# Performance work log

Hardware: AMD Instinct MI355X
Metric: run time of the kernel (lower is better)

## Reference

```python
import jax, jax.numpy as jnp
import numpy as np

B, N, D, P = 4, 4096, 64, 2
M, H = 64, 128
ARENA = 20.0  # positions uniform in [0, ARENA]^2; radius 1.0 -> ~32 neighbors


def _mlp2(x, Wa, ba, Wb, bb):
    return jax.nn.relu(x @ Wa + ba) @ Wb + bb


def setup_inputs() -> dict:
    key = jax.random.key(0)
    ks = jax.random.split(key, 14)
    def lin(k, fan_in, fan_out):
        bound = 1.0 / np.sqrt(fan_in)
        kw, kb = jax.random.split(k)
        W = jax.random.uniform(kw, (fan_in, fan_out), jnp.float32, -bound, bound)
        b = jax.random.uniform(kb, (fan_out,), jnp.float32, -bound, bound)
        return W, b
    W1, b1 = lin(ks[0], D, H)
    W2, b2 = lin(ks[1], H, M)
    W3, b3 = lin(ks[2], 2 * M, H)
    W4, b4 = lin(ks[3], H, M)
    W5, b5 = lin(ks[4], D + M, H)
    W6, b6 = lin(ks[5], H, D)
    agent_states = jax.random.normal(ks[6], (B, N, D), jnp.float32)
    agent_positions = jax.random.uniform(ks[7], (B, N, P), jnp.float32) * ARENA
    return {
        "agent_states": agent_states,
        "agent_positions": agent_positions,
        "neighbor_radius": 1,
        "W1": W1, "b1": b1, "W2": W2, "b2": b2,
        "W3": W3, "b3": b3, "W4": W4, "b4": b4,
        "W5": W5, "b5": b5, "W6": W6, "b6": b6,
    }


def reference(agent_states, agent_positions, neighbor_radius,
              W1, b1, W2, b2, W3, b3, W4, b4, W5, b5, W6, b6):
    n = agent_states.shape[1]
    # message encoder MLP: [B,N,D] -> [B,N,M]
    messages = _mlp2(agent_states, W1, b1, W2, b2)
    # dense pairwise distances [B,N,N] (faithful to original O(N^2) mask)
    diff = agent_positions[:, :, None, :] - agent_positions[:, None, :, :]
    distances = jnp.sqrt(jnp.sum(diff * diff, axis=-1))
    adj = (distances < jnp.float32(neighbor_radius)).astype(messages.dtype)
    adj = adj * (1.0 - jnp.eye(n, dtype=messages.dtype))[None]
    deg = jnp.clip(jnp.sum(adj, axis=-1, keepdims=True), 1.0, None)
    adj = adj / deg
    # vectorized form of the per-agent gather-aggregate loop
    aggregated = jnp.einsum('bij,bjm->bim', adj, messages)
    combined = jnp.concatenate([messages, aggregated], axis=-1)
    final_msgs = _mlp2(combined, W3, b3, W4, b4)
    feats = jnp.concatenate([agent_states, final_msgs], axis=-1)
    out = _mlp2(feats, W5, b5, W6, b6)
    return agent_states + out
```

## Files before the change

### kernel.cpp

```cpp
#include <hip/hip_runtime.h>

typedef unsigned short u16;
typedef __bf16 bf16x8 __attribute__((ext_vector_type(8)));
typedef unsigned short ushort8 __attribute__((ext_vector_type(8)));
typedef float f32x4 __attribute__((ext_vector_type(4)));

#define DEV_INLINE __device__ __forceinline__

constexpr int NB = 4;
constexpr int NAG = 4096;
constexpr int ROWS = NB * NAG;
constexpr int GRID = 20;
constexpr int CELLS = GRID * GRID;
constexpr int CSTRIDE = 404;
constexpr int MAXNB = 320;

DEV_INLINE u16 f2bu(float x) { __bf16 h = (__bf16)x; return __builtin_bit_cast(u16, h); }
DEV_INLINE float bu2f(u16 u) { return __builtin_bit_cast(float, ((unsigned)u) << 16); }

__global__ __launch_bounds__(1024) void setup_kernel(
    const float* __restrict__ pos,
    const float* __restrict__ W1, const float* __restrict__ W2,
    const float* __restrict__ W3, const float* __restrict__ W4,
    const float* __restrict__ W5, const float* __restrict__ W6,
    u16* __restrict__ wts, float2* __restrict__ pos_sorted,
    int* __restrict__ cell_start, int* __restrict__ sid, int* __restrict__ invp)
{
  if (blockIdx.x >= NB) {
    const int idx = (blockIdx.x - NB) * 1024 + threadIdx.x;
    const float* src; int n, k, Nc;
    if (idx < 8192)       { src = W1; int li = idx;          n = li >> 6; k = li & 63;  Nc = 128; }
    else if (idx < 16384) { src = W2; int li = idx - 8192;   n = li >> 7; k = li & 127; Nc = 64;  }
    else if (idx < 32768) { src = W3; int li = idx - 16384;  n = li >> 7; k = li & 127; Nc = 128; }
    else if (idx < 40960) { src = W4; int li = idx - 32768;  n = li >> 7; k = li & 127; Nc = 64;  }
    else if (idx < 57344) { src = W5; int li = idx - 40960;  n = li >> 7; k = li & 127; Nc = 128; }
    else                  { src = W6; int li = idx - 57344;  n = li >> 7; k = li & 127; Nc = 64;  }
    wts[idx] = f2bu(src[k * Nc + n]);
    return;
  }

  __shared__ int cnt_s[CELLS];
  __shared__ int start_s[CELLS + 1];
  __shared__ int scan_s[512];
  __shared__ u16 cell_of[NAG];
  __shared__ u16 rank_of[NAG];

  const int b = blockIdx.x;
  const float2* pb = (const float2*)(pos + (size_t)b * NAG * 2);
  for (int c = threadIdx.x; c < CELLS; c += 1024) cnt_s[c] = 0;
  __syncthreads();

  for (int i = threadIdx.x; i < NAG; i += 1024) {
    float2 p = pb[i];
    int cx = min(max((int)floorf(p.x), 0), GRID - 1);
    int cy = min(max((int)floorf(p.y), 0), GRID - 1);
    int c = cy * GRID + cx;
    int rk = atomicAdd(&cnt_s[c], 1);
    cell_of[i] = (u16)c;
    rank_of[i] = (u16)rk;
  }
  __syncthreads();

  if (threadIdx.x < 512) scan_s[threadIdx.x] = (threadIdx.x < CELLS) ? cnt_s[threadIdx.x] : 0;
  __syncthreads();
  for (int off = 1; off < 512; off <<= 1) {
    int x = 0;
    if (threadIdx.x < 512) {
      x = scan_s[threadIdx.x];
      if (threadIdx.x >= off) x += scan_s[threadIdx.x - off];
    }
    __syncthreads();
    if (threadIdx.x < 512) scan_s[threadIdx.x] = x;
    __syncthreads();
  }
  if (threadIdx.x <= CELLS) {
    int st = (threadIdx.x == 0) ? 0 : scan_s[threadIdx.x - 1];
    start_s[threadIdx.x] = st;
    cell_start[b * CSTRIDE + threadIdx.x] = st;
  }
  __syncthreads();

  for (int i = threadIdx.x; i < NAG; i += 1024) {
    int k = start_s[cell_of[i]] + rank_of[i];
    sid[b * NAG + k]  = b * NAG + i;
    invp[b * NAG + i] = b * NAG + k;
    pos_sorted[b * NAG + k] = pb[i];
  }
}

template<bool BF>
DEV_INLINE bf16x8 loadA(const void* __restrict__ src, int row, int c) {
  if constexpr (BF) {
    ushort8 u = *reinterpret_cast<const ushort8*>((const u16*)src + (size_t)row * 64 + c);
    return __builtin_bit_cast(bf16x8, u);
  } else {
    const float* f = (const float*)src + (size_t)row * 64 + c;
    f32x4 a = *(const f32x4*)f;
    f32x4 b = *(const f32x4*)(f + 4);
    bf16x8 r;
    r[0] = (__bf16)a[0]; r[1] = (__bf16)a[1]; r[2] = (__bf16)a[2]; r[3] = (__bf16)a[3];
    r[4] = (__bf16)b[0]; r[5] = (__bf16)b[1]; r[6] = (__bf16)b[2]; r[7] = (__bf16)b[3];
    return r;
  }
}

template<int KIN, bool A0BF, bool A1BF, bool RESID, bool OUTBF, bool PERM>
__global__ __launch_bounds__(256) void mlp_mfma(
    const void* __restrict__ src0, const void* __restrict__ src1,
    const u16* __restrict__ WaT, const u16* __restrict__ WbT,
    const float* __restrict__ ba, const float* __restrict__ bb,
    const float* __restrict__ resid, const int* __restrict__ perm,
    void* __restrict__ dst)
{
  constexpr int KP = KIN + 8;
  extern __shared__ u16 smem[];
  u16* WaTs = smem;
  u16* WbTs = smem + 128 * KP;
  const int lane = threadIdx.x & 63;
  const int wave = threadIdx.x >> 6;
  u16* hs = WbTs + 64 * 136 + wave * (16 * 136);

  for (int t = threadIdx.x; t < (128 * KIN) / 8; t += 256) {
    int e = t * 8; int n = e / KIN; int k = e - n * KIN;
    *(ushort8*)&WaTs[n * KP + k] = *(const ushort8*)&WaT[e];
  }
  for (int t = threadIdx.x; t < 1024; t += 256) {
    int e = t * 8; int n = e >> 7; int k = e & 127;
    *(ushort8*)&WbTs[n * 136 + k] = *(const ushort8*)&WbT[e];
  }
  __syncthreads();

  const int l15 = lane & 15;
  const int khalf = (lane >> 4) * 8;
  const int rb = blockIdx.x * 64 + wave * 16;
  const int row = rb + l15;

  f32x4 acc1[8] = {};
#pragma unroll
  for (int kt = 0; kt < KIN / 32; ++kt) {
    const int cc = (kt & 1) * 32 + khalf;
    bf16x8 a;
    if constexpr (KIN == 128) {
      if (kt >= 2) a = loadA<A1BF>(src1, row, cc);
      else         a = loadA<A0BF>(src0, row, cc);
    } else {
      a = loadA<A0BF>(src0, row, cc);
    }
#pragma unroll
    for (int nt = 0; nt < 8; ++nt) {
      ushort8 bu = *(const ushort8*)&WaTs[(nt * 16 + l15) * KP + kt * 32 + khalf];
      acc1[nt] = __builtin_amdgcn_mfma_f32_16x16x32_bf16(
          a, __builtin_bit_cast(bf16x8, bu), acc1[nt], 0, 0, 0);
    }
  }

#pragma unroll
  for (int nt = 0; nt < 8; ++nt) {
    const float bav = ba[nt * 16 + l15];
#pragma unroll
    for (int r = 0; r < 4; ++r) {
      float v = acc1[nt][r] + bav;
      v = fmaxf(v, 0.0f);
      hs[((lane >> 4) * 4 + r) * 136 + nt * 16 + l15] = f2bu(v);
    }
  }

  f32x4 acc2[4] = {};
#pragma unroll
  for (int kt = 0; kt < 4; ++kt) {
    ushort8 au = *(const ushort8*)&hs[l15 * 136 + kt * 32 + khalf];
    bf16x8 a2 = __builtin_bit_cast(bf16x8, au);
#pragma unroll
    for (int nt = 0; nt < 4; ++nt) {
      ushort8 bu = *(const ushort8*)&WbTs[(nt * 16 + l15) * 136 + kt * 32 + khalf];
      acc2[nt] = __builtin_amdgcn_mfma_f32_16x16x32_bf16(
          a2, __builtin_bit_cast(bf16x8, bu), acc2[nt], 0, 0, 0);
    }
  }

  int drow[4];
#pragma unroll
  for (int r = 0; r < 4; ++r) {
    const int orow = rb + (lane >> 4) * 4 + r;
    drow[r] = PERM ? perm[orow] : orow;
  }

#pragma unroll
  for (int nt = 0; nt < 4; ++nt) {
    const int gc = nt * 16 + l15;
    const float bbv = bb[gc];
#pragma unroll
    for (int r = 0; r < 4; ++r) {
      const int m = (lane >> 4) * 4 + r;
      const size_t o = (size_t)drow[r] * 64 + gc;
      float v = acc2[nt][r] + bbv;
      if constexpr (RESID) v += resid[(size_t)(rb + m) * 64 + gc];
      if constexpr (OUTBF) ((u16*)dst)[o] = f2bu(v);
      else                 ((float*)dst)[o] = v;
    }
  }
}

__global__ __launch_bounds__(256) void agg_kernel(
    const float2* __restrict__ pos_sorted, const u16* __restrict__ msgs,
    const int* __restrict__ cell_start, const int* __restrict__ radius_ptr,
    u16* __restrict__ aggr)
{
  __shared__ u16 idxb[4][MAXNB];
  const int b = blockIdx.y;
  const int lane = threadIdx.x & 63;
  const int wave = threadIdx.x >> 6;
  const int k = blockIdx.x * 4 + wave;
  const float2* pb = pos_sorted + (size_t)b * NAG;
  const float2 pk = pb[k];
  const float r = (float)(*radius_ptr);
  const float r2 = __fmul_rn(r, r);
  const int cx = min(max((int)floorf(pk.x), 0), GRID - 1);
  const int cy = min(max((int)floorf(pk.y), 0), GRID - 1);
  const int* cs = cell_start + b * CSTRIDE;
  const unsigned long long lt = (1ull << lane) - 1ull;

  int cnt = 0;
#pragma unroll
  for (int dy = -1; dy <= 1; ++dy) {
    const int yy = cy + dy;
    if (yy < 0 || yy >= GRID) continue;
    const int x0 = max(cx - 1, 0), x1 = min(cx + 1, GRID - 1);
    const int c0 = cs[yy * GRID + x0];
    const int c1 = cs[yy * GRID + x1 + 1];
    for (int base = c0; base < c1; base += 64) {
      const int j = base + lane;
      bool ok = false;
      if (j < c1) {
        const float2 pj = pb[j];
        const float dx_ = pk.x - pj.x;
        const float dy_ = pk.y - pj.y;
        const float d2 = __fadd_rn(__fmul_rn(dx_, dx_), __fmul_rn(dy_, dy_));
        ok = (d2 < r2) && (j != k);
      }
      const unsigned long long m = __ballot(ok);
      if (ok) {
        const int p = cnt + __popcll(m & lt);
        if (p < MAXNB) idxb[wave][p] = (u16)j;
      }
      cnt += (int)__popcll(m);
    }
  }

  const u16* mb = msgs + (size_t)b * NAG * 64;
  float acc = 0.0f;
  const int n = min(cnt, MAXNB);
  for (int g = 0; g < n; g += 8) {
    ushort8 ii = *(const ushort8*)&idxb[wave][g];
    float vs[8];
#pragma unroll
    for (int s = 0; s < 8; ++s) {
      const int jj = (g + s < n) ? (int)ii[s] : (int)ii[0];
      vs[s] = bu2f(mb[(size_t)jj * 64 + lane]);
    }
#pragma unroll
    for (int s = 0; s < 8; ++s) acc += (g + s < n) ? vs[s] : 0.0f;
  }
  const float inv = 1.0f / (float)(cnt > 0 ? cnt : 1);
  aggr[((size_t)b * NAG + k) * 64 + lane] = f2bu(acc * inv);
}

extern "C" void kernel_launch(void* const* d_in, const int* in_sizes, int n_in,
                              void* d_out, int out_size, void* d_ws, size_t ws_size,
                              hipStream_t stream) {
  const float* states = (const float*)d_in[0];
  const float* pos    = (const float*)d_in[1];
  const int*   radius = (const int*)d_in[2];
  const float* W1 = (const float*)d_in[3];
  const float* b1 = (const float*)d_in[4];
  const float* W2 = (const float*)d_in[5];
  const float* b2 = (const float*)d_in[6];
  const float* W3 = (const float*)d_in[7];
  const float* b3 = (const float*)d_in[8];
  const float* W4 = (const float*)d_in[9];
  const float* b4 = (const float*)d_in[10];
  const float* W5 = (const float*)d_in[11];
  const float* b5 = (const float*)d_in[12];
  const float* W6 = (const float*)d_in[13];
  const float* b6 = (const float*)d_in[14];
  float* out = (float*)d_out;

  u16* ws16   = (u16*)d_ws;
  u16* msgs   = ws16;
  u16* aggr   = msgs + (size_t)ROWS * 64;
  u16* finalm = aggr + (size_t)ROWS * 64;
  u16* wts    = finalm + (size_t)ROWS * 64;
  char* pbyte = (char*)(wts + 65536);
  float2* pos_sorted = (float2*)pbyte;
  int* cell_start = (int*)(pbyte + (size_t)ROWS * 8);
  int* sid  = cell_start + NB * CSTRIDE;
  int* invp = sid + ROWS;

  constexpr int LDS64  = (128 * 72  + 64 * 136 + 4 * 16 * 136) * 2;
  constexpr int LDS128 = (128 * 136 + 64 * 136 + 4 * 16 * 136) * 2;

  setup_kernel<<<NB + 64, 1024, 0, stream>>>(
      pos, W1, W2, W3, W4, W5, W6, wts, pos_sorted, cell_start, sid, invp);

  mlp_mfma<64, false, false, false, true, true><<<256, 256, LDS64, stream>>>(
      states, nullptr, wts + 0, wts + 8192, b1, b2, nullptr, invp, msgs);

  agg_kernel<<<dim3(NAG / 4, NB), 256, 0, stream>>>(
      pos_sorted, msgs, cell_start, radius, aggr);

  mlp_mfma<128, true, true, false, true, true><<<256, 256, LDS128, stream>>>(
      msgs, aggr, wts + 16384, wts + 32768, b3, b4, nullptr, sid, finalm);

  mlp_mfma<128, false, true, true, false, false><<<256, 256, LDS128, stream>>>(
      states, finalm, wts + 40960, wts + 57344, b5, b6, states, nullptr, out);
}
```

Before: 50.03 us.

## Fuse setup with first MLP and merge final two MLPs into one kernel

The standalone setup kernel is merged into the first MLP launch as extra blocks: spatial binning uses a wave-shuffle scan, and W1/W2 are converted to bf16 directly in LDS. The message buffer stays in original agent order, and the aggregation kernel maps sorted neighbor indices back through sid. The last two MLPs become one kernel that keeps the intermediate final messages in LDS, which removes a launch and the finalm global round trip. In exchange, the fused MLP kernel needs much more LDS, which may lower occupancy, and the gathers in aggregation lose the locality the sorted message order gave them.

```diff
diff --git a/kernel.cpp b/kernel.cpp
--- a/kernel.cpp
+++ b/kernel.cpp
@@ -18,74 +18,9 @@
 DEV_INLINE u16 f2bu(float x) { __bf16 h = (__bf16)x; return __builtin_bit_cast(u16, h); }
 DEV_INLINE float bu2f(u16 u) { return __builtin_bit_cast(float, ((unsigned)u) << 16); }
 
-__global__ __launch_bounds__(1024) void setup_kernel(
-    const float* __restrict__ pos,
-    const float* __restrict__ W1, const float* __restrict__ W2,
-    const float* __restrict__ W3, const float* __restrict__ W4,
-    const float* __restrict__ W5, const float* __restrict__ W6,
-    u16* __restrict__ wts, float2* __restrict__ pos_sorted,
-    int* __restrict__ cell_start, int* __restrict__ sid, int* __restrict__ invp)
-{
-  if (blockIdx.x >= NB) {
-    const int idx = (blockIdx.x - NB) * 1024 + threadIdx.x;
-    const float* src; int n, k, Nc;
-    if (idx < 8192)       { src = W1; int li = idx;          n = li >> 6; k = li & 63;  Nc = 128; }
-    else if (idx < 16384) { src = W2; int li = idx - 8192;   n = li >> 7; k = li & 127; Nc = 64;  }
-    else if (idx < 32768) { src = W3; int li = idx - 16384;  n = li >> 7; k = li & 127; Nc = 128; }
-    else if (idx < 40960) { src = W4; int li = idx - 32768;  n = li >> 7; k = li & 127; Nc = 64;  }
-    else if (idx < 57344) { src = W5; int li = idx - 40960;  n = li >> 7; k = li & 127; Nc = 128; }
-    else                  { src = W6; int li = idx - 57344;  n = li >> 7; k = li & 127; Nc = 64;  }
-    wts[idx] = f2bu(src[k * Nc + n]);
-    return;
-  }
-
-  __shared__ int cnt_s[CELLS];
-  __shared__ int start_s[CELLS + 1];
-  __shared__ int scan_s[512];
-  __shared__ u16 cell_of[NAG];
-  __shared__ u16 rank_of[NAG];
-
-  const int b = blockIdx.x;
-  const float2* pb = (const float2*)(pos + (size_t)b * NAG * 2);
-  for (int c = threadIdx.x; c < CELLS; c += 1024) cnt_s[c] = 0;
-  __syncthreads();
-
-  for (int i = threadIdx.x; i < NAG; i += 1024) {
-    float2 p = pb[i];
-    int cx = min(max((int)floorf(p.x), 0), GRID - 1);
-    int cy = min(max((int)floorf(p.y), 0), GRID - 1);
-    int c = cy * GRID + cx;
-    int rk = atomicAdd(&cnt_s[c], 1);
-    cell_of[i] = (u16)c;
-    rank_of[i] = (u16)rk;
-  }
-  __syncthreads();
-
-  if (threadIdx.x < 512) scan_s[threadIdx.x] = (threadIdx.x < CELLS) ? cnt_s[threadIdx.x] : 0;
-  __syncthreads();
-  for (int off = 1; off < 512; off <<= 1) {
-    int x = 0;
-    if (threadIdx.x < 512) {
-      x = scan_s[threadIdx.x];
-      if (threadIdx.x >= off) x += scan_s[threadIdx.x - off];
-    }
-    __syncthreads();
-    if (threadIdx.x < 512) scan_s[threadIdx.x] = x;
-    __syncthreads();
-  }
-  if (threadIdx.x <= CELLS) {
-    int st = (threadIdx.x == 0) ? 0 : scan_s[threadIdx.x - 1];
-    start_s[threadIdx.x] = st;
-    cell_start[b * CSTRIDE + threadIdx.x] = st;
-  }
-  __syncthreads();
-
-  for (int i = threadIdx.x; i < NAG; i += 1024) {
-    int k = start_s[cell_of[i]] + rank_of[i];
-    sid[b * NAG + k]  = b * NAG + i;
-    invp[b * NAG + i] = b * NAG + k;
-    pos_sorted[b * NAG + k] = pb[i];
-  }
+DEV_INLINE f32x4 MF(bf16x8 a, const u16* p, f32x4 c) {
+  ushort8 bu = *(const ushort8*)p;
+  return __builtin_amdgcn_mfma_f32_16x16x32_bf16(a, __builtin_bit_cast(bf16x8, bu), c, 0, 0, 0);
 }
 
 template<bool BF>
@@ -104,107 +39,138 @@
   }
 }
 
-template<int KIN, bool A0BF, bool A1BF, bool RESID, bool OUTBF, bool PERM>
-__global__ __launch_bounds__(256) void mlp_mfma(
-    const void* __restrict__ src0, const void* __restrict__ src1,
-    const u16* __restrict__ WaT, const u16* __restrict__ WbT,
-    const float* __restrict__ ba, const float* __restrict__ bb,
-    const float* __restrict__ resid, const int* __restrict__ perm,
-    void* __restrict__ dst)
+__global__ __launch_bounds__(256) void fused_setup_mlp1(
+    const float* __restrict__ pos, const float* __restrict__ states,
+    const float* __restrict__ W1, const float* __restrict__ b1,
+    const float* __restrict__ W2, const float* __restrict__ b2,
+    const float* __restrict__ W3, const float* __restrict__ W4,
+    const float* __restrict__ W5, const float* __restrict__ W6,
+    u16* __restrict__ wts, u16* __restrict__ msgs,
+    float2* __restrict__ pos_sorted, int* __restrict__ cell_start,
+    int* __restrict__ sid)
 {
-  constexpr int KP = KIN + 8;
   extern __shared__ u16 smem[];
+  const int tid = threadIdx.x;
+  const int lane = tid & 63;
+  const int wave = tid >> 6;
+
+  if (blockIdx.x < NB) {
+    int* cnt_s = (int*)smem;
+    int* start_s = cnt_s + CELLS;
+    u16* cell_of = (u16*)(start_s + CELLS + 1);
+    u16* rank_of = cell_of + NAG;
+    const int b = blockIdx.x;
+    const float2* pb = (const float2*)(pos + (size_t)b * NAG * 2);
+    for (int c = tid; c < CELLS; c += 256) cnt_s[c] = 0;
+    __syncthreads();
+    for (int i = tid; i < NAG; i += 256) {
+      float2 p = pb[i];
+      int cx = min(max((int)floorf(p.x), 0), GRID - 1);
+      int cy = min(max((int)floorf(p.y), 0), GRID - 1);
+      int c = cy * GRID + cx;
+      rank_of[i] = (u16)atomicAdd(&cnt_s[c], 1);
+      cell_of[i] = (u16)c;
+    }
+    __syncthreads();
+    if (wave == 0) {
+      int carry = 0;
+      for (int g = 0; g < CELLS; g += 64) {
+        int c = g + lane;
+        int x = (c < CELLS) ? cnt_s[c] : 0;
+#pragma unroll
+        for (int off = 1; off < 64; off <<= 1) {
+          int y = __shfl_up(x, off, 64);
+          if (lane >= off) x += y;
+        }
+        if (c < CELLS) start_s[c + 1] = carry + x;
+        carry += __shfl(x, 63, 64);
+      }
+      if (lane == 0) start_s[0] = 0;
+    }
+    __syncthreads();
+    for (int c = tid; c <= CELLS; c += 256) cell_start[b * CSTRIDE + c] = start_s[c];
+    for (int i = tid; i < NAG; i += 256) {
+      int kk = start_s[cell_of[i]] + (int)rank_of[i];
+      sid[b * NAG + kk] = b * NAG + i;
+      pos_sorted[b * NAG + kk] = pb[i];
+    }
+    return;
+  }
+
+  if (blockIdx.x >= NB + 256) {
+    const int base = (blockIdx.x - (NB + 256)) * 3072;
+#pragma unroll
+    for (int t = 0; t < 12; ++t) {
+      int idx = base + t * 256 + tid;
+      const float* src; int n, k, Nc;
+      if (idx < 16384)      { src = W3; n = idx >> 7; k = idx & 127; Nc = 128; }
+      else if (idx < 24576) { int li = idx - 16384; src = W4; n = li >> 7; k = li & 127; Nc = 64; }
+      else if (idx < 40960) { int li = idx - 24576; src = W5; n = li >> 7; k = li & 127; Nc = 128; }
+      else                  { int li = idx - 40960; src = W6; n = li >> 7; k = li & 127; Nc = 64; }
+      wts[idx] = f2bu(src[k * Nc + n]);
+    }
+    return;
+  }
+
   u16* WaTs = smem;
-  u16* WbTs = smem + 128 * KP;
-  const int lane = threadIdx.x & 63;
-  const int wave = threadIdx.x >> 6;
+  u16* WbTs = smem + 128 * 72;
   u16* hs = WbTs + 64 * 136 + wave * (16 * 136);
 
-  for (int t = threadIdx.x; t < (128 * KIN) / 8; t += 256) {
-    int e = t * 8; int n = e / KIN; int k = e - n * KIN;
-    *(ushort8*)&WaTs[n * KP + k] = *(const ushort8*)&WaT[e];
-  }
-  for (int t = threadIdx.x; t < 1024; t += 256) {
-    int e = t * 8; int n = e >> 7; int k = e & 127;
-    *(ushort8*)&WbTs[n * 136 + k] = *(const ushort8*)&WbT[e];
+  for (int e = tid; e < 64 * 128; e += 256) {
+    int n = e & 127, k = e >> 7;
+    WaTs[n * 72 + k] = f2bu(W1[e]);
+  }
+  for (int e = tid; e < 128 * 64; e += 256) {
+    int n = e & 63, k = e >> 6;
+    WbTs[n * 136 + k] = f2bu(W2[e]);
   }
   __syncthreads();
 
   const int l15 = lane & 15;
   const int khalf = (lane >> 4) * 8;
-  const int rb = blockIdx.x * 64 + wave * 16;
+  const int rb = (blockIdx.x - NB) * 64 + wave * 16;
   const int row = rb + l15;
 
   f32x4 acc1[8] = {};
 #pragma unroll
-  for (int kt = 0; kt < KIN / 32; ++kt) {
-    const int cc = (kt & 1) * 32 + khalf;
-    bf16x8 a;
-    if constexpr (KIN == 128) {
-      if (kt >= 2) a = loadA<A1BF>(src1, row, cc);
-      else         a = loadA<A0BF>(src0, row, cc);
-    } else {
-      a = loadA<A0BF>(src0, row, cc);
-    }
-#pragma unroll
-    for (int nt = 0; nt < 8; ++nt) {
-      ushort8 bu = *(const ushort8*)&WaTs[(nt * 16 + l15) * KP + kt * 32 + khalf];
-      acc1[nt] = __builtin_amdgcn_mfma_f32_16x16x32_bf16(
-          a, __builtin_bit_cast(bf16x8, bu), acc1[nt], 0, 0, 0);
-    }
-  }
-
+  for (int kt = 0; kt < 2; ++kt) {
+    bf16x8 a = loadA<false>(states, row, kt * 32 + khalf);
+#pragma unroll
+    for (int nt = 0; nt < 8; ++nt)
+      acc1[nt] = MF(a, &WaTs[(nt * 16 + l15) * 72 + kt * 32 + khalf], acc1[nt]);
+  }
 #pragma unroll
   for (int nt = 0; nt < 8; ++nt) {
-    const float bav = ba[nt * 16 + l15];
-#pragma unroll
-    for (int r = 0; r < 4; ++r) {
-      float v = acc1[nt][r] + bav;
-      v = fmaxf(v, 0.0f);
-      hs[((lane >> 4) * 4 + r) * 136 + nt * 16 + l15] = f2bu(v);
-    }
-  }
-
+    const float bav = b1[nt * 16 + l15];
+#pragma unroll
+    for (int r = 0; r < 4; ++r)
+      hs[((lane >> 4) * 4 + r) * 136 + nt * 16 + l15] = f2bu(fmaxf(acc1[nt][r] + bav, 0.0f));
+  }
   f32x4 acc2[4] = {};
 #pragma unroll
   for (int kt = 0; kt < 4; ++kt) {
     ushort8 au = *(const ushort8*)&hs[l15 * 136 + kt * 32 + khalf];
     bf16x8 a2 = __builtin_bit_cast(bf16x8, au);
 #pragma unroll
-    for (int nt = 0; nt < 4; ++nt) {
-      ushort8 bu = *(const ushort8*)&WbTs[(nt * 16 + l15) * 136 + kt * 32 + khalf];
-      acc2[nt] = __builtin_amdgcn_mfma_f32_16x16x32_bf16(
-          a2, __builtin_bit_cast(bf16x8, bu), acc2[nt], 0, 0, 0);
-    }
-  }
-
-  int drow[4];
-#pragma unroll
-  for (int r = 0; r < 4; ++r) {
-    const int orow = rb + (lane >> 4) * 4 + r;
-    drow[r] = PERM ? perm[orow] : orow;
-  }
-
+    for (int nt = 0; nt < 4; ++nt)
+      acc2[nt] = MF(a2, &WbTs[(nt * 16 + l15) * 136 + kt * 32 + khalf], acc2[nt]);
+  }
 #pragma unroll
   for (int nt = 0; nt < 4; ++nt) {
     const int gc = nt * 16 + l15;
-    const float bbv = bb[gc];
+    const float bbv = b2[gc];
 #pragma unroll
     for (int r = 0; r < 4; ++r) {
       const int m = (lane >> 4) * 4 + r;
-      const size_t o = (size_t)drow[r] * 64 + gc;
-      float v = acc2[nt][r] + bbv;
-      if constexpr (RESID) v += resid[(size_t)(rb + m) * 64 + gc];
-      if constexpr (OUTBF) ((u16*)dst)[o] = f2bu(v);
-      else                 ((float*)dst)[o] = v;
+      msgs[(size_t)(rb + m) * 64 + gc] = f2bu(acc2[nt][r] + bbv);
     }
   }
 }
 
 __global__ __launch_bounds__(256) void agg_kernel(
     const float2* __restrict__ pos_sorted, const u16* __restrict__ msgs,
-    const int* __restrict__ cell_start, const int* __restrict__ radius_ptr,
-    u16* __restrict__ aggr)
+    const int* __restrict__ cell_start, const int* __restrict__ sid,
+    const int* __restrict__ radius_ptr, u16* __restrict__ aggr)
 {
   __shared__ u16 idxb[4][MAXNB];
   const int b = blockIdx.y;
@@ -218,6 +184,7 @@
   const int cx = min(max((int)floorf(pk.x), 0), GRID - 1);
   const int cy = min(max((int)floorf(pk.y), 0), GRID - 1);
   const int* cs = cell_start + b * CSTRIDE;
+  const int* sb = sid + b * NAG;
   const unsigned long long lt = (1ull << lane) - 1ull;
 
   int cnt = 0;
@@ -241,13 +208,12 @@
       const unsigned long long m = __ballot(ok);
       if (ok) {
         const int p = cnt + __popcll(m & lt);
-        if (p < MAXNB) idxb[wave][p] = (u16)j;
+        if (p < MAXNB) idxb[wave][p] = (u16)sb[j];
       }
       cnt += (int)__popcll(m);
     }
   }
 
-  const u16* mb = msgs + (size_t)b * NAG * 64;
   float acc = 0.0f;
   const int n = min(cnt, MAXNB);
   for (int g = 0; g < n; g += 8) {
@@ -256,13 +222,123 @@
 #pragma unroll
     for (int s = 0; s < 8; ++s) {
       const int jj = (g + s < n) ? (int)ii[s] : (int)ii[0];
-      vs[s] = bu2f(mb[(size_t)jj * 64 + lane]);
+      vs[s] = bu2f(msgs[(size_t)jj * 64 + lane]);
     }
 #pragma unroll
     for (int s = 0; s < 8; ++s) acc += (g + s < n) ? vs[s] : 0.0f;
   }
   const float inv = 1.0f / (float)(cnt > 0 ? cnt : 1);
-  aggr[((size_t)b * NAG + k) * 64 + lane] = f2bu(acc * inv);
+  const int orow = sb[k];
+  aggr[(size_t)orow * 64 + lane] = f2bu(acc * inv);
+}
+
+__global__ __launch_bounds__(256) void mlp23_kernel(
+    const float* __restrict__ states, const u16* __restrict__ msgs,
+    const u16* __restrict__ aggr, const u16* __restrict__ wts,
+    const float* __restrict__ b3, const float* __restrict__ b4,
+    const float* __restrict__ b5, const float* __restrict__ b6,
+    float* __restrict__ out)
+{
+  extern __shared__ u16 smem[];
+  u16* W3s = smem;
+  u16* W4s = W3s + 128 * 136;
+  u16* W5s = W4s + 64 * 136;
+  u16* W6s = W5s + 128 * 136;
+  const int tid = threadIdx.x;
+  const int lane = tid & 63;
+  const int wave = tid >> 6;
+  u16* hs = W6s + 64 * 136 + wave * (2 * 16 * 136);
+  u16* fs = hs + 16 * 136;
+
+  for (int t = tid; t < 2048; t += 256) { int e = t * 8; int n = e >> 7, k = e & 127;
+    *(ushort8*)&W3s[n * 136 + k] = *(const ushort8*)&wts[e]; }
+  for (int t = tid; t < 1024; t += 256) { int e = t * 8; int n = e >> 7, k = e & 127;
+    *(ushort8*)&W4s[n * 136 + k] = *(const ushort8*)&wts[16384 + e]; }
+  for (int t = tid; t < 2048; t += 256) { int e = t * 8; int n = e >> 7, k = e & 127;
+    *(ushort8*)&W5s[n * 136 + k] = *(const ushort8*)&wts[24576 + e]; }
+  for (int t = tid; t < 1024; t += 256) { int e = t * 8; int n = e >> 7, k = e & 127;
+    *(ushort8*)&W6s[n * 136 + k] = *(const ushort8*)&wts[40960 + e]; }
+  __syncthreads();
+
+  const int l15 = lane & 15;
+  const int khalf = (lane >> 4) * 8;
+  const int rb = blockIdx.x * 64 + wave * 16;
+  const int row = rb + l15;
+
+  f32x4 acc1[8] = {};
+#pragma unroll
+  for (int kt = 0; kt < 4; ++kt) {
+    const int cc = (kt & 1) * 32 + khalf;
+    bf16x8 a = (kt < 2) ? loadA<true>(msgs, row, cc) : loadA<true>(aggr, row, cc);
+#pragma unroll
+    for (int nt = 0; nt < 8; ++nt)
+      acc1[nt] = MF(a, &W3s[(nt * 16 + l15) * 136 + kt * 32 + khalf], acc1[nt]);
+  }
+#pragma unroll
+  for (int nt = 0; nt < 8; ++nt) {
+    const float bv = b3[nt * 16 + l15];
+#pragma unroll
+    for (int r = 0; r < 4; ++r)
+      hs[((lane >> 4) * 4 + r) * 136 + nt * 16 + l15] = f2bu(fmaxf(acc1[nt][r] + bv, 0.0f));
+  }
+  f32x4 acc2[4] = {};
+#pragma unroll
+  for (int kt = 0; kt < 4; ++kt) {
+    ushort8 au = *(const ushort8*)&hs[l15 * 136 + kt * 32 + khalf];
+    bf16x8 a2 = __builtin_bit_cast(bf16x8, au);
+#pragma unroll
+    for (int nt = 0; nt < 4; ++nt)
+      acc2[nt] = MF(a2, &W4s[(nt * 16 + l15) * 136 + kt * 32 + khalf], acc2[nt]);
+  }
+#pragma unroll
+  for (int nt = 0; nt < 4; ++nt) {
+    const int gc = nt * 16 + l15;
+    const float bv = b4[gc];
+#pragma unroll
+    for (int r = 0; r < 4; ++r)
+      fs[((lane >> 4) * 4 + r) * 136 + gc] = f2bu(acc2[nt][r] + bv);
+  }
+  f32x4 acc3[8] = {};
+#pragma unroll
+  for (int kt = 0; kt < 4; ++kt) {
+    const int cc = (kt & 1) * 32 + khalf;
+    bf16x8 a;
+    if (kt < 2) a = loadA<false>(states, row, cc);
+    else {
+      ushort8 au = *(const ushort8*)&fs[l15 * 136 + cc];
+      a = __builtin_bit_cast(bf16x8, au);
+    }
+#pragma unroll
+    for (int nt = 0; nt < 8; ++nt)
+      acc3[nt] = MF(a, &W5s[(nt * 16 + l15) * 136 + kt * 32 + khalf], acc3[nt]);
+  }
+#pragma unroll
+  for (int nt = 0; nt < 8; ++nt) {
+    const float bv = b5[nt * 16 + l15];
+#pragma unroll
+    for (int r = 0; r < 4; ++r)
+      hs[((lane >> 4) * 4 + r) * 136 + nt * 16 + l15] = f2bu(fmaxf(acc3[nt][r] + bv, 0.0f));
+  }
+  f32x4 acc4[4] = {};
+#pragma unroll
+  for (int kt = 0; kt < 4; ++kt) {
+    ushort8 au = *(const ushort8*)&hs[l15 * 136 + kt * 32 + khalf];
+    bf16x8 a2 = __builtin_bit_cast(bf16x8, au);
+#pragma unroll
+    for (int nt = 0; nt < 4; ++nt)
+      acc4[nt] = MF(a2, &W6s[(nt * 16 + l15) * 136 + kt * 32 + khalf], acc4[nt]);
+  }
+#pragma unroll
+  for (int nt = 0; nt < 4; ++nt) {
+    const int gc = nt * 16 + l15;
+    const float bv = b6[gc];
+#pragma unroll
+    for (int r = 0; r < 4; ++r) {
+      const int m = (lane >> 4) * 4 + r;
+      const size_t o = (size_t)(rb + m) * 64 + gc;
+      out[o] = acc4[nt][r] + bv + states[o];
+    }
+  }
 }
 
 extern "C" void kernel_launch(void* const* d_in, const int* in_sizes, int n_in,
@@ -285,32 +361,25 @@
   const float* b6 = (const float*)d_in[14];
   float* out = (float*)d_out;
 
-  u16* ws16   = (u16*)d_ws;
-  u16* msgs   = ws16;
-  u16* aggr   = msgs + (size_t)ROWS * 64;
-  u16* finalm = aggr + (size_t)ROWS * 64;
-  u16* wts    = finalm + (size_t)ROWS * 64;
-  char* pbyte = (char*)(wts + 65536);
+  u16* ws16 = (u16*)d_ws;
+  u16* msgs = ws16;
+  u16* aggr = msgs + (size_t)ROWS * 64;
+  u16* wts  = aggr + (size_t)ROWS * 64;
+  char* pbyte = (char*)(wts + 49152);
   float2* pos_sorted = (float2*)pbyte;
   int* cell_start = (int*)(pbyte + (size_t)ROWS * 8);
-  int* sid  = cell_start + NB * CSTRIDE;
-  int* invp = sid + ROWS;
-
-  constexpr int LDS64  = (128 * 72  + 64 * 136 + 4 * 16 * 136) * 2;
-  constexpr int LDS128 = (128 * 136 + 64 * 136 + 4 * 16 * 136) * 2;
-
-  setup_kernel<<<NB + 64, 1024, 0, stream>>>(
-      pos, W1, W2, W3, W4, W5, W6, wts, pos_sorted, cell_start, sid, invp);
-
-  mlp_mfma<64, false, false, false, true, true><<<256, 256, LDS64, stream>>>(
-      states, nullptr, wts + 0, wts + 8192, b1, b2, nullptr, invp, msgs);
+  int* sid = cell_start + NB * CSTRIDE;
+
+  constexpr int LDS_K1 = (128 * 72 + 64 * 136 + 4 * 16 * 136) * 2;
+  constexpr int LDS_K3 = (128 * 136 + 64 * 136 + 128 * 136 + 64 * 136 + 4 * 2 * 16 * 136) * 2;
+
+  fused_setup_mlp1<<<NB + 256 + 16, 256, LDS_K1, stream>>>(
+      pos, states, W1, b1, W2, b2, W3, W4, W5, W6,
+      wts, msgs, pos_sorted, cell_start, sid);
 
   agg_kernel<<<dim3(NAG / 4, NB), 256, 0, stream>>>(
-      pos_sorted, msgs, cell_start, radius, aggr);
-
-  mlp_mfma<128, true, true, false, true, true><<<256, 256, LDS128, stream>>>(
-      msgs, aggr, wts + 16384, wts + 32768, b3, b4, nullptr, sid, finalm);
-
-  mlp_mfma<128, false, true, true, false, false><<<256, 256, LDS128, stream>>>(
-      states, finalm, wts + 40960, wts + 57344, b5, b6, states, nullptr, out);
-}
+      pos_sorted, msgs, cell_start, sid, radius, aggr);
+
+  mlp23_kernel<<<256, 256, LDS_K3, stream>>>(
+      states, msgs, aggr, wts, b3, b4, b5, b6, out);
+}
```

After: 43.38 us. 13.3% less time.
